# Kernel optimization log

Hardware: AMD Instinct MI355X
Metric: run time of the kernel (lower is better)

The kernel has to match this reference:

```python
import jax, jax.numpy as jnp
import numpy as np

B, C, H, W = 8, 512, 32, 32


def setup_inputs() -> dict:
    key = jax.random.key(0)
    kx, kq, kk, k6 = jax.random.split(key, 4)
    std = 0.02
    return {
        "x": jax.random.normal(kx, (B, C, H, W), dtype=jnp.float32),
        "Wq": jax.random.normal(kq, (C, C), dtype=jnp.float32) * std,
        "bq": jnp.zeros((C,), dtype=jnp.float32),
        "Wk": jax.random.normal(kk, (C, C), dtype=jnp.float32) * std,
        "bk": jnp.zeros((C,), dtype=jnp.float32),
        "W6": jax.random.normal(k6, (C, C), dtype=jnp.float32) * std,
        "b6": jnp.zeros((C,), dtype=jnp.float32),
    }


def reference(x, Wq, bq, Wk, bk, W6, b6):
    b, c, h, w = x.shape
    hw = h * w
    scale = 1.0 / (c ** 0.5)
    # [B, HW, C] token-major view of the feature map
    xf = jnp.transpose(x.reshape(b, c, hw), (0, 2, 1))
    # 1x1 convs are per-pixel linear layers (weight layout: [C_out, C_in])
    q = xf @ Wq.T + bq                      # [B, HW, C]
    k = xf @ Wk.T + bk                      # [B, HW, C]
    # cross-batch attention scores: every pixel attends to every pixel of every image
    scores = q.reshape(b * hw, c) @ k.reshape(b * hw, c).T   # [B*HW, B*HW]
    s = scores.reshape(b * hw, b, hw)
    # per-query: max response within each image, then mean over images
    xw = jnp.max(s, axis=-1).mean(axis=-1)  # [B*HW]
    xw = xw.reshape(b, hw) * scale
    xw = jax.nn.softmax(xw, axis=-1).reshape(b, 1, h, w)
    x5 = x * xw                             # spatial gating
    # final 1x1 conv
    of = jnp.transpose(x5.reshape(b, c, hw), (0, 2, 1)) @ W6.T + b6
    return jnp.transpose(of, (0, 2, 1)).reshape(b, c, h, w)
```

## Files before the change

### kernel.cpp

```cpp
#include <hip/hip_runtime.h>


typedef __attribute__((ext_vector_type(8))) short bf16x8;
typedef __attribute__((ext_vector_type(4))) float f32x4;
typedef __attribute__((ext_vector_type(2))) long long i64x2;

__device__ __forceinline__ unsigned short f2bf(float f) {
  unsigned u = __builtin_bit_cast(unsigned, f);
  u += 0x7FFFu + ((u >> 16) & 1u);
  return (unsigned short)(u >> 16);
}

__device__ __forceinline__ float bf2f(unsigned short b) {
  return __builtin_bit_cast(float, (unsigned)b << 16);
}

__device__ __forceinline__ unsigned char f2e4m3(float x) {
  unsigned u = __builtin_bit_cast(unsigned, x);
  unsigned char s = (unsigned char)((u >> 24) & 0x80u);
  unsigned a = u & 0x7FFFFFFFu;
  if (a >= 0x43E00000u) return s | 0x7Eu;
  if (a < 0x3C800000u) {
    float q = __builtin_bit_cast(float, a) * 512.f;
    int m = (int)(q + 0.5f);
    return s | (unsigned char)m;
  }
  unsigned r = a + 0x7FFFFu + ((a >> 20) & 1u);
  int e = (int)((r >> 23) & 0xFF) - 127;
  if (e > 8) return s | 0x7Eu;
  unsigned m3 = (r >> 20) & 0x7u;
  return s | (unsigned char)(((e + 7) << 3) | m3);
}

__device__ __forceinline__ void gload_lds16(const void* g, void* l) {
  __builtin_amdgcn_global_load_lds(
      (const __attribute__((address_space(1))) unsigned int*)g,
      (__attribute__((address_space(3))) unsigned int*)l, 16, 0, 0);
}

__global__ __launch_bounds__(256) void prep(const float* __restrict__ x,
                                            const float* __restrict__ Wq,
                                            const float* __restrict__ Wk,
                                            const float* __restrict__ W6,
                                            short* __restrict__ xt,
                                            short* __restrict__ wcat) {
  const int bid = blockIdx.x, u = threadIdx.x;
  if (bid < 1024) {
    const int p0 = (bid & 15) * 64, c0 = ((bid >> 4) & 7) * 64, b = bid >> 7;
    __shared__ float t[64][65];
    {
      const int p4 = u & 15, cr = u >> 4;
      for (int cc = 0; cc < 4; ++cc) {
        const int c = cc * 16 + cr;
        const float4 v = *(const float4*)&x[((size_t)(b * 512 + c0 + c)) * 1024 + p0 + p4 * 4];
        t[p4 * 4 + 0][c] = v.x; t[p4 * 4 + 1][c] = v.y;
        t[p4 * 4 + 2][c] = v.z; t[p4 * 4 + 3][c] = v.w;
      }
    }
    __syncthreads();
    {
      const int c4 = u & 15, pr = u >> 4;
      for (int pp = 0; pp < 4; ++pp) {
        const int p = pp * 16 + pr;
        ushort4 o;
        o.x = f2bf(t[p][c4 * 4 + 0]); o.y = f2bf(t[p][c4 * 4 + 1]);
        o.z = f2bf(t[p][c4 * 4 + 2]); o.w = f2bf(t[p][c4 * 4 + 3]);
        *(ushort4*)&xt[((size_t)(b * 1024 + p0 + p)) * 512 + c0 + c4 * 4] = o;
      }
    }
  } else {
    const int i = (bid - 1024) * 256 + u;
    const int idx = i * 4;
    const float* src = (idx < 262144) ? Wq : (idx < 524288) ? Wk : W6;
    const float4 v = *(const float4*)&src[idx & 262143];
    ushort4 o;
    o.x = f2bf(v.x); o.y = f2bf(v.y); o.z = f2bf(v.z); o.w = f2bf(v.w);
    *(ushort4*)&wcat[idx] = o;
  }
}

__global__ __launch_bounds__(256) void gemm_qkz(const short* __restrict__ xt,
                                                const short* __restrict__ wcat,
                                                const float* __restrict__ bq,
                                                const float* __restrict__ bk,
                                                unsigned char* __restrict__ qk8,
                                                short* __restrict__ z) {
  __shared__ short lds_a[128 * 32];
  __shared__ short lds_b[128 * 32];
  const int tid = threadIdx.x, w = tid >> 6, lane = tid & 63;
  const int wr = w >> 1, wc = w & 1;
  const int quad = lane >> 4, lcol = lane & 15;
  const int srow = lane & 15, skq = lane >> 4;
  const int m0 = blockIdx.x * 128, n0 = blockIdx.y * 128;

  f32x4 acc[4][4];
#pragma unroll
  for (int i = 0; i < 4; ++i)
#pragma unroll
    for (int j = 0; j < 4; ++j)
#pragma unroll
      for (int r = 0; r < 4; ++r) acc[i][j][r] = 0.f;

  const short* Abase = xt + (size_t)(m0 + srow) * 512 + skq * 8;
  const short* Bbase = wcat + (size_t)(n0 + srow) * 512 + skq * 8;

  for (int kt = 0; kt < 16; ++kt) {
    const int kb = kt * 32;
    __syncthreads();
    gload_lds16(Abase + (size_t)(w * 16) * 512 + kb,       lds_a + w * 512);
    gload_lds16(Abase + (size_t)((4 + w) * 16) * 512 + kb, lds_a + (4 + w) * 512);
    gload_lds16(Bbase + (size_t)(w * 16) * 512 + kb,       lds_b + w * 512);
    gload_lds16(Bbase + (size_t)((4 + w) * 16) * 512 + kb, lds_b + (4 + w) * 512);
    __syncthreads();
    bf16x8 af[4], bf[4];
#pragma unroll
    for (int i = 0; i < 4; ++i) af[i] = *(const bf16x8*)&lds_a[(wr * 4 + i) * 512 + lane * 8];
#pragma unroll
    for (int j = 0; j < 4; ++j) bf[j] = *(const bf16x8*)&lds_b[(wc * 4 + j) * 512 + lane * 8];
#pragma unroll
    for (int i = 0; i < 4; ++i)
#pragma unroll
      for (int j = 0; j < 4; ++j)
        acc[i][j] = __builtin_amdgcn_mfma_f32_16x16x32_bf16(af[i], bf[j], acc[i][j], 0, 0, 0);
  }

  const int region = (int)blockIdx.y >> 2;
  if (region < 2) {
    const float* bias = region ? bk : bq;
#pragma unroll
    for (int i = 0; i < 4; ++i)
#pragma unroll
      for (int j = 0; j < 4; ++j) {
        const int row = m0 + wr * 64 + i * 16 + quad * 4;
        const int col = n0 + wc * 64 + j * 16 + lcol;
        const float bv = bias[col & 511];
#pragma unroll
        for (int r = 0; r < 4; ++r)
          qk8[(size_t)(row + r) * 1024 + col] = f2e4m3(acc[i][j][r] + bv);
      }
  } else {
#pragma unroll
    for (int i = 0; i < 4; ++i)
#pragma unroll
      for (int j = 0; j < 4; ++j) {
        const int row = m0 + wr * 64 + i * 16 + quad * 4;
        const int col = n0 - 1024 + wc * 64 + j * 16 + lcol;
#pragma unroll
        for (int r = 0; r < 4; ++r)
          z[(size_t)(row + r) * 512 + col] = (short)f2bf(acc[i][j][r]);
      }
  }
}

__global__ __launch_bounds__(256) void gemm_scores(const unsigned char* __restrict__ qk8,
                                                   float* __restrict__ wsmx) {
  __shared__ unsigned char lds_b[32768];
  const int tid = threadIdx.x, w = tid >> 6, lane = tid & 63;
  const int quad = lane >> 4, lcol = lane & 15;
  const int srow = lane & 15, skb = (lane >> 4) * 16;
  const int m0 = blockIdx.x * 128, n0 = blockIdx.y * 128;

  f32x4 acc[2][8];
#pragma unroll
  for (int rg = 0; rg < 2; ++rg)
#pragma unroll
    for (int j = 0; j < 8; ++j)
#pragma unroll
      for (int r = 0; r < 4; ++r) acc[rg][j][r] = 0.f;

  const unsigned char* Abase = qk8 + (size_t)(m0 + w * 32 + srow) * 1024 + skb;
  const unsigned char* Bbase = qk8 + (size_t)(n0 + srow) * 1024 + 512 + skb;

#pragma unroll
  for (int kh = 0; kh < 2; ++kh) {
    __syncthreads();
#pragma unroll
    for (int jj = 0; jj < 2; ++jj) {
      const int j = w * 2 + jj;
#pragma unroll
      for (int kb = 0; kb < 4; ++kb)
        gload_lds16(Bbase + (size_t)(j * 16) * 1024 + kh * 256 + kb * 64,
                    lds_b + j * 4096 + kb * 1024);
    }
    i64x2 af[2][4];
#pragma unroll
    for (int rg = 0; rg < 2; ++rg)
#pragma unroll
      for (int kb = 0; kb < 4; ++kb)
        af[rg][kb] = *(const i64x2*)(Abase + (size_t)rg * 16384 + kh * 256 + kb * 64);
    __syncthreads();
#pragma unroll
    for (int kb = 0; kb < 4; ++kb) {
#pragma unroll
      for (int j = 0; j < 8; ++j) {
        const i64x2 bf = *(const i64x2*)&lds_b[j * 4096 + kb * 1024 + lane * 16];
#pragma unroll
        for (int rg = 0; rg < 2; ++rg) {
          acc[rg][j] = __builtin_amdgcn_mfma_f32_16x16x32_fp8_fp8(
              af[rg][kb].x, bf.x, acc[rg][j], 0, 0, 0);
          acc[rg][j] = __builtin_amdgcn_mfma_f32_16x16x32_fp8_fp8(
              af[rg][kb].y, bf.y, acc[rg][j], 0, 0, 0);
        }
      }
    }
  }

#pragma unroll
  for (int rg = 0; rg < 2; ++rg) {
#pragma unroll
    for (int r = 0; r < 4; ++r) {
      float v = acc[rg][0][r];
#pragma unroll
      for (int j = 1; j < 8; ++j) v = fmaxf(v, acc[rg][j][r]);
#pragma unroll
      for (int off = 1; off < 16; off <<= 1) v = fmaxf(v, __shfl_xor(v, off));
      if (lcol == 0)
        wsmx[(size_t)blockIdx.y * 8192 + m0 + w * 32 + rg * 16 + quad * 4 + r] = v;
    }
  }
}

__global__ __launch_bounds__(1024) void softmax_xw(const float* __restrict__ wsmx,
                                                   float* __restrict__ xw) {
  const int b = blockIdx.x, p = threadIdx.x;
  const int m = b * 1024 + p;
  float s = 0.f;
#pragma unroll
  for (int img = 0; img < 8; ++img) {
    float mx = -1e30f;
#pragma unroll
    for (int t = 0; t < 8; ++t) mx = fmaxf(mx, wsmx[(size_t)(img * 8 + t) * 8192 + m]);
    s += mx;
  }
  const float logit = s * 0.005524271728019903f;
  __shared__ float red[16];
  float v = logit;
#pragma unroll
  for (int off = 32; off >= 1; off >>= 1) v = fmaxf(v, __shfl_xor(v, off));
  if ((p & 63) == 0) red[p >> 6] = v;
  __syncthreads();
  float bmax = red[0];
#pragma unroll
  for (int t = 1; t < 16; ++t) bmax = fmaxf(bmax, red[t]);
  const float e = expf(logit - bmax);
  float sv = e;
#pragma unroll
  for (int off = 32; off >= 1; off >>= 1) sv += __shfl_xor(sv, off);
  __syncthreads();
  if ((p & 63) == 0) red[p >> 6] = sv;
  __syncthreads();
  float bsum = 0.f;
#pragma unroll
  for (int t = 0; t < 16; ++t) bsum += red[t];
  xw[m] = e / bsum;
}

__global__ __launch_bounds__(256) void epilogue_out(const short* __restrict__ z,
                                                    const float* __restrict__ xw,
                                                    const float* __restrict__ b6,
                                                    float* __restrict__ out) {
  const int p0 = blockIdx.x * 64, c0 = blockIdx.y * 64, b = blockIdx.z;
  __shared__ float t[64][65];
  const int u = threadIdx.x;
  {
    const int c4 = u & 15, pr = u >> 4;
    for (int pp = 0; pp < 4; ++pp) {
      const int p = pp * 16 + pr;
      const ushort4 v = *(const ushort4*)&z[((size_t)(b * 1024 + p0 + p)) * 512 + c0 + c4 * 4];
      t[c4 * 4 + 0][p] = bf2f(v.x);
      t[c4 * 4 + 1][p] = bf2f(v.y);
      t[c4 * 4 + 2][p] = bf2f(v.z);
      t[c4 * 4 + 3][p] = bf2f(v.w);
    }
  }
  __syncthreads();
  {
    const int p4 = u & 15, cr = u >> 4;
    const float4 wv = *(const float4*)&xw[b * 1024 + p0 + p4 * 4];
    for (int cc = 0; cc < 4; ++cc) {
      const int co = cc * 16 + cr;
      const float bias = b6[c0 + co];
      float4 o;
      o.x = t[co][p4 * 4 + 0] * wv.x + bias;
      o.y = t[co][p4 * 4 + 1] * wv.y + bias;
      o.z = t[co][p4 * 4 + 2] * wv.z + bias;
      o.w = t[co][p4 * 4 + 3] * wv.w + bias;
      *(float4*)&out[((size_t)(b * 512 + c0 + co)) * 1024 + p0 + p4 * 4] = o;
    }
  }
}

extern "C" void kernel_launch(void* const* d_in, const int* in_sizes, int n_in,
                              void* d_out, int out_size, void* d_ws, size_t ws_size,
                              hipStream_t stream) {
  const float* x  = (const float*)d_in[0];
  const float* Wq = (const float*)d_in[1];
  const float* bq = (const float*)d_in[2];
  const float* Wk = (const float*)d_in[3];
  const float* bk = (const float*)d_in[4];
  const float* W6 = (const float*)d_in[5];
  const float* b6 = (const float*)d_in[6];
  float* out = (float*)d_out;

  char* ws = (char*)d_ws;
  short* xt          = (short*)(ws + 0);
  short* wcat        = (short*)(ws + 8388608);
  unsigned char* qk8 = (unsigned char*)(ws + 10485760);
  short* z           = (short*)(ws + 18874368);
  float* wsmx        = (float*)(ws + 27262976);
  float* xw          = (float*)(ws + 29360128);

  prep<<<1792, 256, 0, stream>>>(x, Wq, Wk, W6, xt, wcat);
  gemm_qkz<<<dim3(64, 12), 256, 0, stream>>>(xt, wcat, bq, bk, qk8, z);
  gemm_scores<<<dim3(64, 64), 256, 0, stream>>>(qk8, wsmx);
  softmax_xw<<<8, 1024, 0, stream>>>(wsmx, xw);
  epilogue_out<<<dim3(16, 8, 8), 256, 0, stream>>>(z, xw, b6, out);
}
```

Before: 191.7 us.

## Restructure QKZ GEMM: register-resident A fragments, larger K staging, hardware fp8 convert

The QK/Z projection GEMM now has each wave own 32 rows and all 128 columns. A fragments are loaded straight from global memory into registers, and only B is staged in LDS, in 128-wide K chunks. This cuts the number of barriers from 32 to 8 and removes the A shared-memory round trip. The software e4m3 conversion is replaced with the hardware cvt_pk_fp8_f32 instruction. In exchange the kernel uses more LDS (32KB) and more registers, and rounding or saturation may differ slightly from the hand-written converter.

Measured after the change: 181.8 us. 5.2% less time.

```diff
diff --git a/kernel.cpp b/kernel.cpp
--- a/kernel.cpp
+++ b/kernel.cpp
@@ -13,23 +13,6 @@
 
 __device__ __forceinline__ float bf2f(unsigned short b) {
   return __builtin_bit_cast(float, (unsigned)b << 16);
-}
-
-__device__ __forceinline__ unsigned char f2e4m3(float x) {
-  unsigned u = __builtin_bit_cast(unsigned, x);
-  unsigned char s = (unsigned char)((u >> 24) & 0x80u);
-  unsigned a = u & 0x7FFFFFFFu;
-  if (a >= 0x43E00000u) return s | 0x7Eu;
-  if (a < 0x3C800000u) {
-    float q = __builtin_bit_cast(float, a) * 512.f;
-    int m = (int)(q + 0.5f);
-    return s | (unsigned char)m;
-  }
-  unsigned r = a + 0x7FFFFu + ((a >> 20) & 1u);
-  int e = (int)((r >> 23) & 0xFF) - 127;
-  if (e > 8) return s | 0x7Eu;
-  unsigned m3 = (r >> 20) & 0x7u;
-  return s | (unsigned char)(((e + 7) << 3) | m3);
 }
 
 __device__ __forceinline__ void gload_lds16(const void* g, void* l) {
@@ -85,70 +68,86 @@
                                                 const float* __restrict__ bk,
                                                 unsigned char* __restrict__ qk8,
                                                 short* __restrict__ z) {
-  __shared__ short lds_a[128 * 32];
-  __shared__ short lds_b[128 * 32];
+  __shared__ short lds_b[16384];
   const int tid = threadIdx.x, w = tid >> 6, lane = tid & 63;
-  const int wr = w >> 1, wc = w & 1;
   const int quad = lane >> 4, lcol = lane & 15;
   const int srow = lane & 15, skq = lane >> 4;
   const int m0 = blockIdx.x * 128, n0 = blockIdx.y * 128;
 
-  f32x4 acc[4][4];
-#pragma unroll
-  for (int i = 0; i < 4; ++i)
-#pragma unroll
-    for (int j = 0; j < 4; ++j)
-#pragma unroll
-      for (int r = 0; r < 4; ++r) acc[i][j][r] = 0.f;
-
-  const short* Abase = xt + (size_t)(m0 + srow) * 512 + skq * 8;
+  f32x4 acc[2][8];
+#pragma unroll
+  for (int rg = 0; rg < 2; ++rg)
+#pragma unroll
+    for (int j = 0; j < 8; ++j)
+#pragma unroll
+      for (int r = 0; r < 4; ++r) acc[rg][j][r] = 0.f;
+
+  const short* Abase = xt + (size_t)(m0 + w * 32 + srow) * 512 + skq * 8;
   const short* Bbase = wcat + (size_t)(n0 + srow) * 512 + skq * 8;
 
-  for (int kt = 0; kt < 16; ++kt) {
-    const int kb = kt * 32;
-    __syncthreads();
-    gload_lds16(Abase + (size_t)(w * 16) * 512 + kb,       lds_a + w * 512);
-    gload_lds16(Abase + (size_t)((4 + w) * 16) * 512 + kb, lds_a + (4 + w) * 512);
-    gload_lds16(Bbase + (size_t)(w * 16) * 512 + kb,       lds_b + w * 512);
-    gload_lds16(Bbase + (size_t)((4 + w) * 16) * 512 + kb, lds_b + (4 + w) * 512);
-    __syncthreads();
-    bf16x8 af[4], bf[4];
-#pragma unroll
-    for (int i = 0; i < 4; ++i) af[i] = *(const bf16x8*)&lds_a[(wr * 4 + i) * 512 + lane * 8];
-#pragma unroll
-    for (int j = 0; j < 4; ++j) bf[j] = *(const bf16x8*)&lds_b[(wc * 4 + j) * 512 + lane * 8];
-#pragma unroll
-    for (int i = 0; i < 4; ++i)
-#pragma unroll
-      for (int j = 0; j < 4; ++j)
-        acc[i][j] = __builtin_amdgcn_mfma_f32_16x16x32_bf16(af[i], bf[j], acc[i][j], 0, 0, 0);
+#pragma unroll
+  for (int kh = 0; kh < 4; ++kh) {
+    const int ke = kh * 128;
+    __syncthreads();
+#pragma unroll
+    for (int jj = 0; jj < 2; ++jj) {
+      const int j = w * 2 + jj;
+#pragma unroll
+      for (int kb = 0; kb < 4; ++kb)
+        gload_lds16(Bbase + (size_t)(j * 16) * 512 + ke + kb * 32,
+                    lds_b + j * 2048 + kb * 512);
+    }
+    bf16x8 af[2][4];
+#pragma unroll
+    for (int rg = 0; rg < 2; ++rg)
+#pragma unroll
+      for (int kb = 0; kb < 4; ++kb)
+        af[rg][kb] = *(const bf16x8*)(Abase + (size_t)rg * 16 * 512 + ke + kb * 32);
+    __syncthreads();
+#pragma unroll
+    for (int kb = 0; kb < 4; ++kb) {
+#pragma unroll
+      for (int j = 0; j < 8; ++j) {
+        const bf16x8 bf = *(const bf16x8*)&lds_b[j * 2048 + kb * 512 + lane * 8];
+#pragma unroll
+        for (int rg = 0; rg < 2; ++rg)
+          acc[rg][j] = __builtin_amdgcn_mfma_f32_16x16x32_bf16(af[rg][kb], bf, acc[rg][j], 0, 0, 0);
+      }
+    }
   }
 
   const int region = (int)blockIdx.y >> 2;
   if (region < 2) {
     const float* bias = region ? bk : bq;
 #pragma unroll
-    for (int i = 0; i < 4; ++i)
-#pragma unroll
-      for (int j = 0; j < 4; ++j) {
-        const int row = m0 + wr * 64 + i * 16 + quad * 4;
-        const int col = n0 + wc * 64 + j * 16 + lcol;
+    for (int rg = 0; rg < 2; ++rg) {
+      const int row = m0 + w * 32 + rg * 16 + quad * 4;
+#pragma unroll
+      for (int j = 0; j < 8; ++j) {
+        const int col = n0 + j * 16 + lcol;
         const float bv = bias[col & 511];
+        const int p01 = __builtin_amdgcn_cvt_pk_fp8_f32(
+            acc[rg][j][0] + bv, acc[rg][j][1] + bv, 0, false);
+        const int p23 = __builtin_amdgcn_cvt_pk_fp8_f32(
+            acc[rg][j][2] + bv, acc[rg][j][3] + bv, 0, false);
+        qk8[(size_t)(row + 0) * 1024 + col] = (unsigned char)(p01 & 0xFF);
+        qk8[(size_t)(row + 1) * 1024 + col] = (unsigned char)((p01 >> 8) & 0xFF);
+        qk8[(size_t)(row + 2) * 1024 + col] = (unsigned char)(p23 & 0xFF);
+        qk8[(size_t)(row + 3) * 1024 + col] = (unsigned char)((p23 >> 8) & 0xFF);
+      }
+    }
+  } else {
+#pragma unroll
+    for (int rg = 0; rg < 2; ++rg) {
+      const int row = m0 + w * 32 + rg * 16 + quad * 4;
+#pragma unroll
+      for (int j = 0; j < 8; ++j) {
+        const int col = n0 - 1024 + j * 16 + lcol;
 #pragma unroll
         for (int r = 0; r < 4; ++r)
-          qk8[(size_t)(row + r) * 1024 + col] = f2e4m3(acc[i][j][r] + bv);
-      }
-  } else {
-#pragma unroll
-    for (int i = 0; i < 4; ++i)
-#pragma unroll
-      for (int j = 0; j < 4; ++j) {
-        const int row = m0 + wr * 64 + i * 16 + quad * 4;
-        const int col = n0 - 1024 + wc * 64 + j * 16 + lcol;
-#pragma unroll
-        for (int r = 0; r < 4; ++r)
-          z[(size_t)(row + r) * 512 + col] = (short)f2bf(acc[i][j][r]);
-      }
+          z[(size_t)(row + r) * 512 + col] = (short)f2bf(acc[rg][j][r]);
+      }
+    }
   }
 }
 
```
